# Optimization experiments

Hardware: AMD Instinct MI355X
Metric: run time of the kernel (lower is better)

The kernel has to match this reference:

```python
import jax, jax.numpy as jnp
import numpy as np

N_NODES = 20000
N_EDGES = 640000
HIDDEN = 128
NUM_FILTERS = 128
NUM_RBF = 50
NUM_LAYERS = 6
MAX_Z = 100
CUTOFF_UPPER = 5.0
CUTOFF_LOWER = 0.0


def _cosine_cutoff(d):
    # torchmd CosineCutoff with cutoff_lower == 0
    c = 0.5 * (jnp.cos(d * jnp.pi / CUTOFF_UPPER) + 1.0)
    return c * (d < CUTOFF_UPPER).astype(d.dtype)


def setup_inputs() -> dict:
    key = jax.random.key(0)
    ks = jax.random.split(key, 16)
    s = 0.05
    z = jax.random.randint(ks[0], (N_NODES,), 0, MAX_Z)
    pos = jax.random.uniform(ks[1], (N_NODES, 3), dtype=jnp.float32) * 3.0
    src = jax.random.randint(ks[2], (N_EDGES,), 0, N_NODES)
    off = jax.random.randint(ks[3], (N_EDGES,), 1, N_NODES)
    dst = (src + off) % N_NODES  # no self loops -> d > 0 a.s.
    edge_index = jnp.stack([src, dst])
    batch = jnp.zeros((N_NODES,), dtype=jnp.int32)
    # expnorm RBF initial params (ExpNormalSmearing._initial_params)
    start = float(np.exp(-CUTOFF_UPPER + CUTOFF_LOWER))
    rbf_means = jnp.linspace(start, 1.0, NUM_RBF, dtype=jnp.float32)
    rbf_betas = jnp.full((NUM_RBF,), (2.0 / NUM_RBF * (1.0 - start)) ** -2, dtype=jnp.float32)

    def w(k, shape):
        return jax.random.normal(k, shape, dtype=jnp.float32) * s

    L = NUM_LAYERS
    return dict(
        z=z, pos=pos, edge_index=edge_index, batch=batch,
        emb_table=w(ks[4], (MAX_Z, HIDDEN)),
        nbr_emb_table=w(ks[5], (MAX_Z, HIDDEN)),
        nbr_proj_W=w(ks[6], (NUM_RBF, HIDDEN)),
        nbr_proj_b=jnp.zeros((HIDDEN,), jnp.float32),
        combine_W=w(ks[7], (2 * HIDDEN, HIDDEN)),
        combine_b=jnp.zeros((HIDDEN,), jnp.float32),
        rbf_means=rbf_means, rbf_betas=rbf_betas,
        mlp_W1=w(ks[8], (L, NUM_RBF, NUM_FILTERS)),
        mlp_b1=jnp.zeros((L, NUM_FILTERS), jnp.float32),
        mlp_W2=w(ks[9], (L, NUM_FILTERS, NUM_FILTERS)),
        mlp_b2=jnp.zeros((L, NUM_FILTERS), jnp.float32),
        lin1_W=w(ks[10], (L, HIDDEN, NUM_FILTERS)),
        lin2_W=w(ks[11], (L, NUM_FILTERS, HIDDEN)),
        lin2_b=jnp.zeros((L, HIDDEN), jnp.float32),
        lin_W=w(ks[12], (L, HIDDEN, HIDDEN)),
        lin_b=jnp.zeros((L, HIDDEN), jnp.float32),
    )


def reference(z, pos, edge_index, batch, emb_table, nbr_emb_table,
              nbr_proj_W, nbr_proj_b, combine_W, combine_b,
              rbf_means, rbf_betas,
              mlp_W1, mlp_b1, mlp_W2, mlp_b2,
              lin1_W, lin2_W, lin2_b, lin_W, lin_b):
    src, dst = edge_index[0], edge_index[1]
    # Distance (loop=False): edge_vec = pos[src] - pos[dst]
    vec = pos[src] - pos[dst]                      # [E, 3]
    d = jnp.sqrt(jnp.sum(vec * vec, axis=-1))      # [E]
    C = _cosine_cutoff(d)                          # [E]
    alpha = 5.0 / (CUTOFF_UPPER - CUTOFF_LOWER)
    # ExpNormalSmearing: C(d) * exp(-beta * (exp(alpha*(-d+low)) - mu)^2)
    edge_attr = C[:, None] * jnp.exp(
        -rbf_betas * (jnp.exp(alpha * (-d[:, None] + CUTOFF_LOWER)) - rbf_means) ** 2
    )                                              # [E, R]
    x = emb_table[z]                               # [N, H]
    # NeighborEmbedding (self-loop edges masked out, add aggregation)
    nl_mask = (src != dst).astype(x.dtype)
    Wn = (edge_attr @ nbr_proj_W + nbr_proj_b) * (C * nl_mask)[:, None]  # [E, H]
    xn = nbr_emb_table[z]
    agg = jax.ops.segment_sum(xn[src] * Wn, dst, num_segments=N_NODES)
    x = jnp.concatenate([x, agg], axis=1) @ combine_W + combine_b

    def layer(xc, p):
        W1, b1, W2, b2, l1W, l2W, l2b, lW, lb = p
        # CFConv filter: MLP(edge_attr) * cosine_cutoff
        Wf = (jax.nn.silu(edge_attr @ W1 + b1) @ W2 + b2) * C[:, None]   # [E, F]
        h = xc @ l1W                                                      # [N, F]
        ag = jax.ops.segment_sum(h[src] * Wf, dst, num_segments=N_NODES)  # scatter-add
        h = jax.nn.silu(ag @ l2W + l2b)
        h = h @ lW + lb
        return xc + h, None

    x, _ = jax.lax.scan(layer, x, (mlp_W1, mlp_b1, mlp_W2, mlp_b2,
                                   lin1_W, lin2_W, lin2_b, lin_W, lin_b))
    return x
```

## Files before the change

kernel.cpp:

```cpp
#include <hip/hip_runtime.h>
#include <hip/hip_bf16.h>
#include <math.h>

#define NN 20000
#define NE 640000
#define H  128
#define RB 50
#define NL 6
#define TBINS 4096
#define WBLK (128 * 136)
#define NEPAD (NE + 2 * NN + 64)

typedef unsigned short u16;
typedef __attribute__((ext_vector_type(8))) short short8v;
typedef __attribute__((ext_vector_type(4))) float f32x4;

__device__ __forceinline__ u16 f2b(float v) {
  unsigned x = __float_as_uint(v);
  unsigned r = (x + 0x7FFFu + ((x >> 16) & 1u)) >> 16;
  return (u16)r;
}
__device__ __forceinline__ float b2f(u16 u) {
  return __uint_as_float(((unsigned int)u) << 16);
}

__global__ void k_hist(const int* __restrict__ ei, int* __restrict__ counts) {
  int e = blockIdx.x * blockDim.x + threadIdx.x;
  if (e < NE) atomicAdd(&counts[ei[NE + e]], 1);
}
__global__ __launch_bounds__(1024) void k_scan(const int* __restrict__ counts,
                                               int* __restrict__ pstart,
                                               int* __restrict__ cursorP) {
  __shared__ int tsum[1024];
  int tid = threadIdx.x;
  int base = tid * 20;
  int s = 0;
  #pragma unroll
  for (int j = 0; j < 20; ++j) {
    int i = base + j;
    if (i < NN) { int c = counts[i]; s += ((c + 2) / 3) * 3; }
  }
  tsum[tid] = s;
  __syncthreads();
  for (int off = 1; off < 1024; off <<= 1) {
    int t = (tid >= off) ? tsum[tid - off] : 0;
    __syncthreads();
    tsum[tid] += t;
    __syncthreads();
  }
  int run = (tid > 0) ? tsum[tid - 1] : 0;
  #pragma unroll
  for (int j = 0; j < 20; ++j) {
    int i = base + j;
    if (i < NN) {
      pstart[i] = run; cursorP[i] = run;
      int c = counts[i];
      run += ((c + 2) / 3) * 3;
    }
  }
}
__global__ void k_fill(int* __restrict__ perm) {
  int i = blockIdx.x * blockDim.x + threadIdx.x;
  if (i < NEPAD) perm[i] = -1;
}
__global__ void k_place(const int* __restrict__ ei, int* __restrict__ cursorP,
                        int* __restrict__ perm) {
  int e = blockIdx.x * blockDim.x + threadIdx.x;
  if (e < NE) {
    int t = ei[NE + e];
    int p = atomicAdd(&cursorP[t], 1);
    perm[p] = e;
  }
}
__global__ void k_edge(const int* __restrict__ perm, const int* __restrict__ ei,
                       const float* __restrict__ pos,
                       int* __restrict__ srcS, float* __restrict__ tvS) {
  int p = blockIdx.x * 256 + threadIdx.x;
  if (p >= NEPAD) return;
  int e = perm[p];
  int s = 0;
  float tv = expf(-5.f);
  if (e >= 0) {
    s = ei[e];
    int t = ei[NE + e];
    float dx = pos[3*s]   - pos[3*t];
    float dy = pos[3*s+1] - pos[3*t+1];
    float dz = pos[3*s+2] - pos[3*t+2];
    float d = sqrtf(dx*dx + dy*dy + dz*dz);
    tv = expf(-d);
  }
  srcS[p] = s;
  tvS[p] = tv;
}

__global__ __launch_bounds__(256) void k_tbuild(
    const float* __restrict__ means, const float* __restrict__ betas,
    const float* __restrict__ npW, const float* __restrict__ npb,
    const float* __restrict__ W1, const float* __restrict__ b1,
    const float* __restrict__ W2, const float* __restrict__ b2,
    u16* __restrict__ tbp)
{
  int t  = blockIdx.x / (TBINS / 32);
  int j0 = (blockIdx.x % (TBINS / 32)) * 32;
  __shared__ float sAttr[32][52];
  __shared__ float sCut[32];
  __shared__ float sT[32][132];
  int tid = threadIdx.x;
  float tv0 = expf(-5.f);
  float dtv = (1.f - tv0) / (float)(TBINS - 1);
  for (int idx = tid; idx < 32 * RB; idx += 256) {
    int r = idx / RB, k = idx % RB;
    float tv = tv0 + (j0 + r) * dtv;
    float d = -logf(tv);
    float C = 0.5f * (cosf(d * 0.628318530717958647692f) + 1.f);
    if (d >= 5.f) C = 0.f;
    float diff = tv - means[k];
    sAttr[r][k] = C * expf(-betas[k] * diff * diff);
    if (k == 0) sCut[r] = C;
  }
  __syncthreads();
  int g = tid >> 5, c0 = (tid & 31) * 4, eb = g * 4;
  float acc[4][4];
  #pragma unroll
  for (int i = 0; i < 4; ++i)
    for (int j = 0; j < 4; ++j) acc[i][j] = 0.f;
  const float* Wa = (t == 0) ? npW : (W1 + (size_t)(t - 1) * RB * H);
  for (int k = 0; k < RB; ++k) {
    float4 wv = *(const float4*)&Wa[(size_t)k * H + c0];
    #pragma unroll
    for (int i = 0; i < 4; ++i) {
      float a = sAttr[eb + i][k];
      acc[i][0] += a * wv.x; acc[i][1] += a * wv.y;
      acc[i][2] += a * wv.z; acc[i][3] += a * wv.w;
    }
  }
  size_t obase = (size_t)t * TBINS * 256;
  float fout[4][4];
  if (t == 0) {
    float4 b4 = *(const float4*)&npb[c0];
    float bvA[4] = {b4.x, b4.y, b4.z, b4.w};
    #pragma unroll
    for (int i = 0; i < 4; ++i) {
      float Cv = sCut[eb + i];
      #pragma unroll
      for (int j = 0; j < 4; ++j) fout[i][j] = (acc[i][j] + bvA[j]) * Cv;
    }
  } else {
    float4 b4 = *(const float4*)&b1[(size_t)(t - 1) * H + c0];
    float bvA[4] = {b4.x, b4.y, b4.z, b4.w};
    #pragma unroll
    for (int i = 0; i < 4; ++i) {
      #pragma unroll
      for (int j = 0; j < 4; ++j) {
        float v = acc[i][j] + bvA[j];
        sT[eb + i][c0 + j] = v / (1.f + __expf(-v));
      }
    }
    __syncthreads();
    #pragma unroll
    for (int i = 0; i < 4; ++i)
      for (int j = 0; j < 4; ++j) acc[i][j] = 0.f;
    const float* Wb = W2 + (size_t)(t - 1) * H * H;
    for (int k = 0; k < H; ++k) {
      float4 wv = *(const float4*)&Wb[(size_t)k * H + c0];
      #pragma unroll
      for (int i = 0; i < 4; ++i) {
        float a = sT[eb + i][k];
        acc[i][0] += a * wv.x; acc[i][1] += a * wv.y;
        acc[i][2] += a * wv.z; acc[i][3] += a * wv.w;
      }
    }
    float4 b24 = *(const float4*)&b2[(size_t)(t - 1) * H + c0];
    float bvB[4] = {b24.x, b24.y, b24.z, b24.w};
    #pragma unroll
    for (int i = 0; i < 4; ++i) {
      float Cv = sCut[eb + i];
      #pragma unroll
      for (int j = 0; j < 4; ++j) fout[i][j] = (acc[i][j] + bvB[j]) * Cv;
    }
  }
  #pragma unroll
  for (int i = 0; i < 4; ++i) {
    int jrow = j0 + eb + i;
    #pragma unroll
    for (int j = 0; j < 4; ++j) {
      int c = c0 + j;
      u16 v = f2b(fout[i][j]);
      int g16 = c & 15, slot = c >> 4;
      tbp[obase + ((size_t)jrow * 16 + g16) * 16 + slot] = v;
      if (jrow >= 1)
        tbp[obase + ((size_t)(jrow - 1) * 16 + g16) * 16 + 8 + slot] = v;
    }
  }
}

__global__ void k_prepw2(const float* __restrict__ l2W, const float* __restrict__ lW,
                         const float* __restrict__ l1W, const float* __restrict__ cW,
                         u16* __restrict__ wt) {
  int i = blockIdx.x * 256 + threadIdx.x;
  if (i >= (3 * NL + 2) * WBLK) return;
  if (i < 3 * NL * WBLK) {
    int a = i / (NL * WBLK);
    int r = i % (NL * WBLK);
    int l = r / WBLK;
    int r2 = r % WBLK;
    int n = r2 / 136, k = r2 % 136;
    const float* src = (a == 0) ? l2W : (a == 1) ? lW : l1W;
    wt[i] = (k < H) ? f2b(src[(size_t)l * H * H + (size_t)k * H + n]) : (u16)0;
  } else {
    int j = i - 3 * NL * WBLK;
    int which = j / WBLK;
    int r2 = j % WBLK;
    int n = r2 / 136, k = r2 % 136;
    wt[i] = (k < H) ? f2b(cW[(size_t)(which * 128 + k) * H + n]) : (u16)0;
  }
}

__global__ void k_embed(const int* __restrict__ z, const float* __restrict__ emb,
                        const float* __restrict__ nemb,
                        float* __restrict__ x, u16* __restrict__ xnb) {
  int i = blockIdx.x * blockDim.x + threadIdx.x;
  if (i >= NN * H) return;
  int n = i >> 7, c = i & (H - 1);
  long o = (long)z[n] * H + c;
  x[i] = emb[o];
  xnb[(size_t)n * H + ((c & 15) * 8 + (c >> 4))] = f2b(nemb[o]);
}

__global__ __launch_bounds__(256) void k_eso(
    const int* __restrict__ counts, const int* __restrict__ pstart,
    const int* __restrict__ srcS, const float* __restrict__ tvS,
    const u16* __restrict__ tbp, const u16* __restrict__ hsrc,
    float* __restrict__ agg, int maskSelf)
{
  int tid = threadIdx.x;
  int n = blockIdx.x * 16 + (tid >> 4);
  int r16 = tid & 15;
  int cnt = counts[n];
  int cntp = ((cnt + 2) / 3) * 3;
  long e0 = (long)pstart[n];
  float tv0 = expf(-5.f);
  float inv = (float)(TBINS - 1) / (1.f - tv0);
  float vsum[8];
  #pragma unroll
  for (int ct = 0; ct < 8; ++ct) vsum[ct] = 0.f;
  int P0_s, P1_s, P2_s;
  float P0_w, P1_w, P2_w;
  short8v P0_hv, P0_lo, P0_hi, P1_hv, P1_lo, P1_hi, P2_hv, P2_lo, P2_hi;
#define ISSUE(P, ii) { \
    long e = e0 + (ii); \
    P##_s = srcS[e]; float tvv = tvS[e]; \
    P##_hv = *(const short8v*)&hsrc[(size_t)P##_s * H + r16 * 8]; \
    float u = fminf(fmaxf((tvv - tv0) * inv, 0.f), (float)(TBINS - 1) - 1e-3f); \
    int jj = (int)u; P##_w = u - (float)jj; \
    const u16* tp = &tbp[((size_t)jj * 16 + r16) * 16]; \
    P##_lo = *(const short8v*)tp; \
    P##_hi = *(const short8v*)(tp + 8); }
#define CONSUME(P) { \
    float m = (maskSelf && P##_s == n) ? 0.f : 1.f; \
    _Pragma("unroll") \
    for (int ct = 0; ct < 8; ++ct) { \
      float lo = b2f((u16)P##_lo[ct]); \
      float hi = b2f((u16)P##_hi[ct]); \
      vsum[ct] += (lo + P##_w * (hi - lo)) * m * b2f((u16)P##_hv[ct]); \
    } }
  ISSUE(P0, 0); ISSUE(P1, 1); ISSUE(P2, 2);
  for (int i = 0; i < cntp; i += 3) {
    CONSUME(P0); ISSUE(P0, i + 3);
    CONSUME(P1); ISSUE(P1, i + 4);
    CONSUME(P2); ISSUE(P2, i + 5);
  }
#undef ISSUE
#undef CONSUME
  float* ap = agg + (size_t)n * H + r16;
  #pragma unroll
  for (int ct = 0; ct < 8; ++ct) ap[ct * 16] = vsum[ct];
}

__global__ __launch_bounds__(256) void k_combineM(
    const float* __restrict__ xb, const float* __restrict__ ag,
    const u16* __restrict__ cWt0, const u16* __restrict__ cWt1,
    const float* __restrict__ cb, const u16* __restrict__ l1W0t,
    float* __restrict__ xout, u16* __restrict__ hb)
{
  __shared__ __align__(16) u16 sX[64 * 136];
  __shared__ __align__(16) u16 sG[64 * 136];
  int tid = threadIdx.x;
  int lane = tid & 63, wv = tid >> 6;
  int r16 = lane & 15, g4 = lane >> 4;
  int n0 = blockIdx.x * 64;
  #pragma unroll
  for (int j = 0; j < 8; ++j) {
    int f4 = tid + j * 256;
    int r = f4 >> 5, c4 = f4 & 31;
    int n = n0 + r;
    float4 vx = make_float4(0.f, 0.f, 0.f, 0.f);
    float4 vg = make_float4(0.f, 0.f, 0.f, 0.f);
    if (n < NN) {
      vx = *(const float4*)&xb[(size_t)n * H + c4 * 4];
      vg = *(const float4*)&ag[(size_t)n * H + c4 * 4];
    }
    *(unsigned*)&sX[r * 136 + c4 * 4]     = (unsigned)f2b(vx.x) | ((unsigned)f2b(vx.y) << 16);
    *(unsigned*)&sX[r * 136 + c4 * 4 + 2] = (unsigned)f2b(vx.z) | ((unsigned)f2b(vx.w) << 16);
    *(unsigned*)&sG[r * 136 + c4 * 4]     = (unsigned)f2b(vg.x) | ((unsigned)f2b(vg.y) << 16);
    *(unsigned*)&sG[r * 136 + c4 * 4 + 2] = (unsigned)f2b(vg.z) | ((unsigned)f2b(vg.w) << 16);
  }
  __syncthreads();
  int wrow = wv * 16;
  f32x4 acc[8];
  #pragma unroll
  for (int ct = 0; ct < 8; ++ct) acc[ct] = (f32x4){0.f, 0.f, 0.f, 0.f};
  #pragma unroll
  for (int kt = 0; kt < 4; ++kt) {
    short8v aF = *(const short8v*)&sX[(wrow + r16) * 136 + kt * 32 + g4 * 8];
    #pragma unroll
    for (int ct = 0; ct < 8; ++ct) {
      short8v bF = *(const short8v*)&cWt0[(ct * 16 + r16) * 136 + kt * 32 + g4 * 8];
      acc[ct] = __builtin_amdgcn_mfma_f32_16x16x32_bf16(aF, bF, acc[ct], 0, 0, 0);
    }
  }
  #pragma unroll
  for (int kt = 0; kt < 4; ++kt) {
    short8v aF = *(const short8v*)&sG[(wrow + r16) * 136 + kt * 32 + g4 * 8];
    #pragma unroll
    for (int ct = 0; ct < 8; ++ct) {
      short8v bF = *(const short8v*)&cWt1[(ct * 16 + r16) * 136 + kt * 32 + g4 * 8];
      acc[ct] = __builtin_amdgcn_mfma_f32_16x16x32_bf16(aF, bF, acc[ct], 0, 0, 0);
    }
  }
  #pragma unroll
  for (int ct = 0; ct < 8; ++ct) {
    float bb = cb[ct * 16 + r16];
    #pragma unroll
    for (int r = 0; r < 4; ++r) {
      int n = n0 + wrow + g4 * 4 + r;
      if (n < NN) {
        float o = acc[ct][r] + bb;
        xout[(size_t)n * H + ct * 16 + r16] = o;
        sX[(wrow + g4 * 4 + r) * 136 + ct * 16 + r16] = f2b(o);
      }
    }
  }
  #pragma unroll
  for (int ct = 0; ct < 8; ++ct) acc[ct] = (f32x4){0.f, 0.f, 0.f, 0.f};
  #pragma unroll
  for (int kt = 0; kt < 4; ++kt) {
    short8v aF = *(const short8v*)&sX[(wrow + r16) * 136 + kt * 32 + g4 * 8];
    #pragma unroll
    for (int ct = 0; ct < 8; ++ct) {
      short8v bF = *(const short8v*)&l1W0t[(ct * 16 + r16) * 136 + kt * 32 + g4 * 8];
      acc[ct] = __builtin_amdgcn_mfma_f32_16x16x32_bf16(aF, bF, acc[ct], 0, 0, 0);
    }
  }
  #pragma unroll
  for (int r = 0; r < 4; ++r) {
    int n = n0 + wrow + g4 * 4 + r;
    if (n < NN) {
      short8v hv;
      #pragma unroll
      for (int ct = 0; ct < 8; ++ct) hv[ct] = (short)f2b(acc[ct][r]);
      *(short8v*)&hb[(size_t)n * H + r16 * 8] = hv;
    }
  }
}

__global__ __launch_bounds__(128) void k_gemmM(
    const float* __restrict__ A, const u16* __restrict__ W2t, const float* __restrict__ b2,
    const u16* __restrict__ W3t, const float* __restrict__ b3,
    const float* __restrict__ xin, float* __restrict__ xout,
    const u16* __restrict__ l1Wnt, u16* __restrict__ hb)
{
  __shared__ __align__(16) u16 sA[32 * 136];
  __shared__ __align__(16) u16 sT[32 * 136];
  int tid = threadIdx.x;
  int lane = tid & 63, wv = tid >> 6;
  int r16 = lane & 15, g4 = lane >> 4;
  int n0 = blockIdx.x * 32;
  #pragma unroll
  for (int j = 0; j < 8; ++j) {
    int f4 = tid + j * 128;
    int r = f4 >> 5, c4 = f4 & 31;
    float4 v = *(const float4*)&A[(size_t)(n0 + r) * H + c4 * 4];
    *(unsigned*)&sA[r * 136 + c4 * 4]     = (unsigned)f2b(v.x) | ((unsigned)f2b(v.y) << 16);
    *(unsigned*)&sA[r * 136 + c4 * 4 + 2] = (unsigned)f2b(v.z) | ((unsigned)f2b(v.w) << 16);
  }
  __syncthreads();
  int wrow = wv * 16;
  f32x4 acc[8];
  #pragma unroll
  for (int ct = 0; ct < 8; ++ct) acc[ct] = (f32x4){0.f, 0.f, 0.f, 0.f};
  #pragma unroll
  for (int kt = 0; kt < 4; ++kt) {
    short8v aF = *(const short8v*)&sA[(wrow + r16) * 136 + kt * 32 + g4 * 8];
    #pragma unroll
    for (int ct = 0; ct < 8; ++ct) {
      short8v bF = *(const short8v*)&W2t[(ct * 16 + r16) * 136 + kt * 32 + g4 * 8];
      acc[ct] = __builtin_amdgcn_mfma_f32_16x16x32_bf16(aF, bF, acc[ct], 0, 0, 0);
    }
  }
  #pragma unroll
  for (int ct = 0; ct < 8; ++ct) {
    float bb = b2[ct * 16 + r16];
    #pragma unroll
    for (int r = 0; r < 4; ++r) {
      float v = acc[ct][r] + bb;
      v = v / (1.f + __expf(-v));
      sT[(wrow + g4 * 4 + r) * 136 + ct * 16 + r16] = f2b(v);
    }
  }
  #pragma unroll
  for (int ct = 0; ct < 8; ++ct) acc[ct] = (f32x4){0.f, 0.f, 0.f, 0.f};
  #pragma unroll
  for (int kt = 0; kt < 4; ++kt) {
    short8v aF = *(const short8v*)&sT[(wrow + r16) * 136 + kt * 32 + g4 * 8];
    #pragma unroll
    for (int ct = 0; ct < 8; ++ct) {
      short8v bF = *(const short8v*)&W3t[(ct * 16 + r16) * 136 + kt * 32 + g4 * 8];
      acc[ct] = __builtin_amdgcn_mfma_f32_16x16x32_bf16(aF, bF, acc[ct], 0, 0, 0);
    }
  }
  #pragma unroll
  for (int ct = 0; ct < 8; ++ct) {
    float bb = b3[ct * 16 + r16];
    #pragma unroll
    for (int r = 0; r < 4; ++r) {
      int n = n0 + wrow + g4 * 4 + r;
      float o = acc[ct][r] + bb + xin[(size_t)n * H + ct * 16 + r16];
      xout[(size_t)n * H + ct * 16 + r16] = o;
      sA[(wrow + g4 * 4 + r) * 136 + ct * 16 + r16] = f2b(o);
    }
  }
  if (!l1Wnt) return;
  #pragma unroll
  for (int ct = 0; ct < 8; ++ct) acc[ct] = (f32x4){0.f, 0.f, 0.f, 0.f};
  #pragma unroll
  for (int kt = 0; kt < 4; ++kt) {
    short8v aF = *(const short8v*)&sA[(wrow + r16) * 136 + kt * 32 + g4 * 8];
    #pragma unroll
    for (int ct = 0; ct < 8; ++ct) {
      short8v bF = *(const short8v*)&l1Wnt[(ct * 16 + r16) * 136 + kt * 32 + g4 * 8];
      acc[ct] = __builtin_amdgcn_mfma_f32_16x16x32_bf16(aF, bF, acc[ct], 0, 0, 0);
    }
  }
  #pragma unroll
  for (int r = 0; r < 4; ++r) {
    int n = n0 + wrow + g4 * 4 + r;
    short8v hv;
    #pragma unroll
    for (int ct = 0; ct < 8; ++ct) hv[ct] = (short)f2b(acc[ct][r]);
    *(short8v*)&hb[(size_t)n * H + r16 * 8] = hv;
  }
}

extern "C" void kernel_launch(void* const* d_in, const int* in_sizes, int n_in,
                              void* d_out, int out_size, void* d_ws, size_t ws_size,
                              hipStream_t stream) {
  int bo = (n_in >= 4 && in_sizes[3] == NN) ? 0 : -1;
  const int*   z     = (const int*)d_in[0];
  const float* pos   = (const float*)d_in[1];
  const int*   ei    = (const int*)d_in[2];
  const float* emb   = (const float*)d_in[4 + bo];
  const float* nemb  = (const float*)d_in[5 + bo];
  const float* npW   = (const float*)d_in[6 + bo];
  const float* npb   = (const float*)d_in[7 + bo];
  const float* cW    = (const float*)d_in[8 + bo];
  const float* cb    = (const float*)d_in[9 + bo];
  const float* means = (const float*)d_in[10 + bo];
  const float* betas = (const float*)d_in[11 + bo];
  const float* W1    = (const float*)d_in[12 + bo];
  const float* b1    = (const float*)d_in[13 + bo];
  const float* W2    = (const float*)d_in[14 + bo];
  const float* b2    = (const float*)d_in[15 + bo];
  const float* l1W   = (const float*)d_in[16 + bo];
  const float* l2W   = (const float*)d_in[17 + bo];
  const float* l2b   = (const float*)d_in[18 + bo];
  const float* lW    = (const float*)d_in[19 + bo];
  const float* lb    = (const float*)d_in[20 + bo];

  char* w = (char*)d_ws;
  auto alloc = [&](size_t bytes) { char* p = w; w += (bytes + 255) & ~(size_t)255; return p; };
  int*   counts  = (int*)  alloc((size_t)NN * 4);
  int*   pstart  = (int*)  alloc((size_t)NN * 4);
  int*   cursorP = (int*)  alloc((size_t)NN * 4);
  int*   perm    = (int*)  alloc((size_t)NEPAD * 4);
  int*   srcS    = (int*)  alloc((size_t)NEPAD * 4);
  float* tvS     = (float*)alloc((size_t)NEPAD * 4);
  u16*   tbp     = (u16*)  alloc((size_t)7 * TBINS * 256 * 2);
  u16*   wt      = (u16*)  alloc((size_t)(3 * NL + 2) * WBLK * 2);
  float* xbuf    = (float*)alloc((size_t)NN * H * 4);
  float* agg     = (float*)alloc((size_t)NN * H * 4);
  u16*   xnb     = (u16*)  alloc((size_t)NN * H * 2);
  u16*   hbA     = (u16*)  alloc((size_t)NN * H * 2);
  u16*   hbB     = (u16*)  alloc((size_t)NN * H * 2);

  u16* l2Wt = wt;
  u16* lWt  = wt + (size_t)NL * WBLK;
  u16* l1Wt = wt + (size_t)2 * NL * WBLK;
  u16* cWt0 = wt + (size_t)3 * NL * WBLK;
  u16* cWt1 = cWt0 + WBLK;

  dim3 b256(256);
  int gE256 = (NE + 255) / 256;
  int gNH   = (NN * H + 255) / 256;
  int gNEP  = (NEPAD + 255) / 256;
  int gESO  = NN / 16;
  int gC    = (NN + 63) / 64;
  int gM    = NN / 32;
  int gTB   = 7 * (TBINS / 32);
  int gPW   = ((3 * NL + 2) * WBLK + 255) / 256;

  hipMemsetAsync(counts, 0, (size_t)NN * 4, stream);
  k_hist<<<gE256, b256, 0, stream>>>(ei, counts);
  k_scan<<<1, 1024, 0, stream>>>(counts, pstart, cursorP);
  k_fill<<<gNEP, b256, 0, stream>>>(perm);
  k_place<<<gE256, b256, 0, stream>>>(ei, cursorP, perm);
  k_edge<<<gNEP, b256, 0, stream>>>(perm, ei, pos, srcS, tvS);
  k_tbuild<<<gTB, b256, 0, stream>>>(means, betas, npW, npb, W1, b1, W2, b2, tbp);
  k_prepw2<<<gPW, b256, 0, stream>>>(l2W, lW, l1W, cW, wt);
  k_embed<<<gNH, b256, 0, stream>>>(z, emb, nemb, xbuf, xnb);

  k_eso<<<gESO, b256, 0, stream>>>(counts, pstart, srcS, tvS, tbp, xnb, agg, 1);
  k_combineM<<<gC, b256, 0, stream>>>(xbuf, agg, cWt0, cWt1, cb, l1Wt, xbuf, hbA);

  u16* hin = hbA;
  u16* hout = hbB;
  for (int l = 0; l < NL; ++l) {
    k_eso<<<gESO, b256, 0, stream>>>(counts, pstart, srcS, tvS,
                                     tbp + (size_t)(1 + l) * TBINS * 256,
                                     hin, agg, 0);
    const u16* l1Wnt = (l + 1 < NL) ? (l1Wt + (size_t)(l + 1) * WBLK) : nullptr;
    float* xo = (l == NL - 1) ? (float*)d_out : xbuf;
    k_gemmM<<<gM, dim3(128), 0, stream>>>(agg, l2Wt + (size_t)l * WBLK, l2b + (size_t)l * H,
                                          lWt + (size_t)l * WBLK, lb + (size_t)l * H,
                                          xbuf, xo, l1Wnt, hout);
    u16* tmp = hin; hin = hout; hout = tmp;
  }
}
```

Before: 592.3 us.

## Split each node's edge list across two thread groups and compact filter table

The edge-gather kernel now gives each destination node two 16-thread groups, each covering half of its padded edge range. The halves write separate partial aggregation buffers, which the combine and GEMM kernels add on load. The filter lookup table drops the duplicated lo/hi interleaved layout and stores one row per bin, so each lookup reads two adjacent rows. The aim is more parallelism and shorter per-thread dependency chains in the gather, plus half the table footprint. The cost is an extra NN×H float buffer written and read each layer.

```diff
diff --git a/kernel.cpp b/kernel.cpp
--- a/kernel.cpp
+++ b/kernel.cpp
@@ -98,7 +98,7 @@
     const float* __restrict__ npW, const float* __restrict__ npb,
     const float* __restrict__ W1, const float* __restrict__ b1,
     const float* __restrict__ W2, const float* __restrict__ b2,
-    u16* __restrict__ tbp)
+    u16* __restrict__ tb)
 {
   int t  = blockIdx.x / (TBINS / 32);
   int j0 = (blockIdx.x % (TBINS / 32)) * 32;
@@ -134,16 +134,18 @@
       acc[i][2] += a * wv.z; acc[i][3] += a * wv.w;
     }
   }
-  size_t obase = (size_t)t * TBINS * 256;
-  float fout[4][4];
+  size_t obase = (size_t)t * TBINS * H;
+  int pb = (c0 & 15) * 8 + (c0 >> 4);
   if (t == 0) {
     float4 b4 = *(const float4*)&npb[c0];
     float bvA[4] = {b4.x, b4.y, b4.z, b4.w};
     #pragma unroll
     for (int i = 0; i < 4; ++i) {
       float Cv = sCut[eb + i];
+      size_t rb = obase + (size_t)(j0 + eb + i) * H;
       #pragma unroll
-      for (int j = 0; j < 4; ++j) fout[i][j] = (acc[i][j] + bvA[j]) * Cv;
+      for (int j = 0; j < 4; ++j)
+        tb[rb + pb + 8 * j] = f2b((acc[i][j] + bvA[j]) * Cv);
     }
   } else {
     float4 b4 = *(const float4*)&b1[(size_t)(t - 1) * H + c0];
@@ -175,21 +177,10 @@
     #pragma unroll
     for (int i = 0; i < 4; ++i) {
       float Cv = sCut[eb + i];
+      size_t rb = obase + (size_t)(j0 + eb + i) * H;
       #pragma unroll
-      for (int j = 0; j < 4; ++j) fout[i][j] = (acc[i][j] + bvB[j]) * Cv;
-    }
-  }
-  #pragma unroll
-  for (int i = 0; i < 4; ++i) {
-    int jrow = j0 + eb + i;
-    #pragma unroll
-    for (int j = 0; j < 4; ++j) {
-      int c = c0 + j;
-      u16 v = f2b(fout[i][j]);
-      int g16 = c & 15, slot = c >> 4;
-      tbp[obase + ((size_t)jrow * 16 + g16) * 16 + slot] = v;
-      if (jrow >= 1)
-        tbp[obase + ((size_t)(jrow - 1) * 16 + g16) * 16 + 8 + slot] = v;
+      for (int j = 0; j < 4; ++j)
+        tb[rb + pb + 8 * j] = f2b((acc[i][j] + bvB[j]) * Cv);
     }
   }
 }
@@ -230,14 +221,18 @@
 __global__ __launch_bounds__(256) void k_eso(
     const int* __restrict__ counts, const int* __restrict__ pstart,
     const int* __restrict__ srcS, const float* __restrict__ tvS,
-    const u16* __restrict__ tbp, const u16* __restrict__ hsrc,
-    float* __restrict__ agg, int maskSelf)
+    const u16* __restrict__ tb, const u16* __restrict__ hsrc,
+    float* __restrict__ agg0, float* __restrict__ agg1, int maskSelf)
 {
   int tid = threadIdx.x;
-  int n = blockIdx.x * 16 + (tid >> 4);
-  int r16 = tid & 15;
+  int grp = tid >> 4, r16 = tid & 15;
+  int n = blockIdx.x * 8 + (grp >> 1);
+  int half = grp & 1;
   int cnt = counts[n];
   int cntp = ((cnt + 2) / 3) * 3;
+  int h0 = (((cntp / 3) + 1) / 2) * 3;
+  int lo = half ? h0 : 0;
+  int hi = half ? cntp : h0;
   long e0 = (long)pstart[n];
   float tv0 = expf(-5.f);
   float inv = (float)(TBINS - 1) / (1.f - tv0);
@@ -253,32 +248,32 @@
     P##_hv = *(const short8v*)&hsrc[(size_t)P##_s * H + r16 * 8]; \
     float u = fminf(fmaxf((tvv - tv0) * inv, 0.f), (float)(TBINS - 1) - 1e-3f); \
     int jj = (int)u; P##_w = u - (float)jj; \
-    const u16* tp = &tbp[((size_t)jj * 16 + r16) * 16]; \
-    P##_lo = *(const short8v*)tp; \
-    P##_hi = *(const short8v*)(tp + 8); }
+    P##_lo = *(const short8v*)&tb[(size_t)jj * H + r16 * 8]; \
+    P##_hi = *(const short8v*)&tb[((size_t)jj + 1) * H + r16 * 8]; }
 #define CONSUME(P) { \
     float m = (maskSelf && P##_s == n) ? 0.f : 1.f; \
     _Pragma("unroll") \
     for (int ct = 0; ct < 8; ++ct) { \
-      float lo = b2f((u16)P##_lo[ct]); \
-      float hi = b2f((u16)P##_hi[ct]); \
-      vsum[ct] += (lo + P##_w * (hi - lo)) * m * b2f((u16)P##_hv[ct]); \
+      float lo2 = b2f((u16)P##_lo[ct]); \
+      float hi2 = b2f((u16)P##_hi[ct]); \
+      vsum[ct] += (lo2 + P##_w * (hi2 - lo2)) * m * b2f((u16)P##_hv[ct]); \
     } }
-  ISSUE(P0, 0); ISSUE(P1, 1); ISSUE(P2, 2);
-  for (int i = 0; i < cntp; i += 3) {
+  ISSUE(P0, lo); ISSUE(P1, lo + 1); ISSUE(P2, lo + 2);
+  for (int i = lo; i < hi; i += 3) {
     CONSUME(P0); ISSUE(P0, i + 3);
     CONSUME(P1); ISSUE(P1, i + 4);
     CONSUME(P2); ISSUE(P2, i + 5);
   }
 #undef ISSUE
 #undef CONSUME
-  float* ap = agg + (size_t)n * H + r16;
+  float* ap = (half ? agg1 : agg0) + (size_t)n * H + r16;
   #pragma unroll
   for (int ct = 0; ct < 8; ++ct) ap[ct * 16] = vsum[ct];
 }
 
 __global__ __launch_bounds__(256) void k_combineM(
-    const float* __restrict__ xb, const float* __restrict__ ag,
+    const float* __restrict__ xb, const float* __restrict__ ag0,
+    const float* __restrict__ ag1,
     const u16* __restrict__ cWt0, const u16* __restrict__ cWt1,
     const float* __restrict__ cb, const u16* __restrict__ l1W0t,
     float* __restrict__ xout, u16* __restrict__ hb)
@@ -298,7 +293,10 @@
     float4 vg = make_float4(0.f, 0.f, 0.f, 0.f);
     if (n < NN) {
       vx = *(const float4*)&xb[(size_t)n * H + c4 * 4];
-      vg = *(const float4*)&ag[(size_t)n * H + c4 * 4];
+      float4 g0 = *(const float4*)&ag0[(size_t)n * H + c4 * 4];
+      float4 g1 = *(const float4*)&ag1[(size_t)n * H + c4 * 4];
+      vg.x = g0.x + g1.x; vg.y = g0.y + g1.y;
+      vg.z = g0.z + g1.z; vg.w = g0.w + g1.w;
     }
     *(unsigned*)&sX[r * 136 + c4 * 4]     = (unsigned)f2b(vx.x) | ((unsigned)f2b(vx.y) << 16);
     *(unsigned*)&sX[r * 136 + c4 * 4 + 2] = (unsigned)f2b(vx.z) | ((unsigned)f2b(vx.w) << 16);
@@ -365,7 +363,8 @@
 }
 
 __global__ __launch_bounds__(128) void k_gemmM(
-    const float* __restrict__ A, const u16* __restrict__ W2t, const float* __restrict__ b2,
+    const float* __restrict__ A0, const float* __restrict__ A1,
+    const u16* __restrict__ W2t, const float* __restrict__ b2,
     const u16* __restrict__ W3t, const float* __restrict__ b3,
     const float* __restrict__ xin, float* __restrict__ xout,
     const u16* __restrict__ l1Wnt, u16* __restrict__ hb)
@@ -380,7 +379,9 @@
   for (int j = 0; j < 8; ++j) {
     int f4 = tid + j * 128;
     int r = f4 >> 5, c4 = f4 & 31;
-    float4 v = *(const float4*)&A[(size_t)(n0 + r) * H + c4 * 4];
+    float4 v0 = *(const float4*)&A0[(size_t)(n0 + r) * H + c4 * 4];
+    float4 v1 = *(const float4*)&A1[(size_t)(n0 + r) * H + c4 * 4];
+    float4 v = make_float4(v0.x + v1.x, v0.y + v1.y, v0.z + v1.z, v0.w + v1.w);
     *(unsigned*)&sA[r * 136 + c4 * 4]     = (unsigned)f2b(v.x) | ((unsigned)f2b(v.y) << 16);
     *(unsigned*)&sA[r * 136 + c4 * 4 + 2] = (unsigned)f2b(v.z) | ((unsigned)f2b(v.w) << 16);
   }
@@ -485,10 +486,11 @@
   int*   perm    = (int*)  alloc((size_t)NEPAD * 4);
   int*   srcS    = (int*)  alloc((size_t)NEPAD * 4);
   float* tvS     = (float*)alloc((size_t)NEPAD * 4);
-  u16*   tbp     = (u16*)  alloc((size_t)7 * TBINS * 256 * 2);
+  u16*   tb      = (u16*)  alloc((size_t)7 * TBINS * H * 2);
   u16*   wt      = (u16*)  alloc((size_t)(3 * NL + 2) * WBLK * 2);
   float* xbuf    = (float*)alloc((size_t)NN * H * 4);
-  float* agg     = (float*)alloc((size_t)NN * H * 4);
+  float* agg0    = (float*)alloc((size_t)NN * H * 4);
+  float* agg1    = (float*)alloc((size_t)NN * H * 4);
   u16*   xnb     = (u16*)  alloc((size_t)NN * H * 2);
   u16*   hbA     = (u16*)  alloc((size_t)NN * H * 2);
   u16*   hbB     = (u16*)  alloc((size_t)NN * H * 2);
@@ -503,7 +505,7 @@
   int gE256 = (NE + 255) / 256;
   int gNH   = (NN * H + 255) / 256;
   int gNEP  = (NEPAD + 255) / 256;
-  int gESO  = NN / 16;
+  int gESO  = NN / 8;
   int gC    = (NN + 63) / 64;
   int gM    = NN / 32;
   int gTB   = 7 * (TBINS / 32);
@@ -515,22 +517,23 @@
   k_fill<<<gNEP, b256, 0, stream>>>(perm);
   k_place<<<gE256, b256, 0, stream>>>(ei, cursorP, perm);
   k_edge<<<gNEP, b256, 0, stream>>>(perm, ei, pos, srcS, tvS);
-  k_tbuild<<<gTB, b256, 0, stream>>>(means, betas, npW, npb, W1, b1, W2, b2, tbp);
+  k_tbuild<<<gTB, b256, 0, stream>>>(means, betas, npW, npb, W1, b1, W2, b2, tb);
   k_prepw2<<<gPW, b256, 0, stream>>>(l2W, lW, l1W, cW, wt);
   k_embed<<<gNH, b256, 0, stream>>>(z, emb, nemb, xbuf, xnb);
 
-  k_eso<<<gESO, b256, 0, stream>>>(counts, pstart, srcS, tvS, tbp, xnb, agg, 1);
-  k_combineM<<<gC, b256, 0, stream>>>(xbuf, agg, cWt0, cWt1, cb, l1Wt, xbuf, hbA);
+  k_eso<<<gESO, b256, 0, stream>>>(counts, pstart, srcS, tvS, tb, xnb, agg0, agg1, 1);
+  k_combineM<<<gC, b256, 0, stream>>>(xbuf, agg0, agg1, cWt0, cWt1, cb, l1Wt, xbuf, hbA);
 
   u16* hin = hbA;
   u16* hout = hbB;
   for (int l = 0; l < NL; ++l) {
     k_eso<<<gESO, b256, 0, stream>>>(counts, pstart, srcS, tvS,
-                                     tbp + (size_t)(1 + l) * TBINS * 256,
-                                     hin, agg, 0);
+                                     tb + (size_t)(1 + l) * TBINS * H,
+                                     hin, agg0, agg1, 0);
     const u16* l1Wnt = (l + 1 < NL) ? (l1Wt + (size_t)(l + 1) * WBLK) : nullptr;
     float* xo = (l == NL - 1) ? (float*)d_out : xbuf;
-    k_gemmM<<<gM, dim3(128), 0, stream>>>(agg, l2Wt + (size_t)l * WBLK, l2b + (size_t)l * H,
+    k_gemmM<<<gM, dim3(128), 0, stream>>>(agg0, agg1,
+                                          l2Wt + (size_t)l * WBLK, l2b + (size_t)l * H,
                                           lWt + (size_t)l * WBLK, lb + (size_t)l * H,
                                           xbuf, xo, l1Wnt, hout);
     u16* tmp = hin; hin = hout; hout = tmp;
```

Measured after the change: 574.5 us. 3.0% less time.
